# Performance work log

Hardware: AMD Instinct MI355X
Metric: run time of the kernel (lower is better)

Reference implementation:

```python
import jax, jax.numpy as jnp
import numpy as np

B, T, C, H = 4, 2048, 1024, 8
D = C // H


def _rope_tables(t, d, base=10000.0):
    inv = 1.0 / (base ** (jnp.arange(0, d, 2, dtype=jnp.float32) / d))
    freqs = jnp.outer(jnp.arange(t, dtype=jnp.float32), inv)  # (T, D/2)
    cos = jnp.concatenate([jnp.cos(freqs)] * 2, axis=-1)  # (T, D)
    sin = jnp.concatenate([jnp.sin(freqs)] * 2, axis=-1)
    return cos, sin


def _apply_rope(x, cos, sin):
    # x: (B,H,T,D); rotate-half RoPE
    d2 = x.shape[-1] // 2
    x1, x2 = x[..., :d2], x[..., d2:]
    rot = jnp.concatenate([-x2, x1], axis=-1)
    return x * cos + rot * sin


def setup_inputs() -> dict:
    key = jax.random.key(0)
    ks = jax.random.split(key, 8)
    x = jax.random.normal(ks[0], (B, T, C), jnp.float32)
    w = lambda k: jax.random.normal(k, (C, C), jnp.float32) * 0.02
    # trigram directions: 8 sign patterns in {-1,+1}^3, L2-normalized (as in get_trigrams + F.normalize)
    signs = np.array([[(1 if (i >> b) & 1 else -1) for b in range(3)] for i in range(8)], np.float32)
    head_dirs = jnp.asarray(signs / np.sqrt(3.0))
    return {
        'x': x,
        'Wq': w(ks[1]), 'Wk': w(ks[2]), 'Wv': w(ks[3]), 'Wo': w(ks[4]),
        'ln_g': jnp.ones((C,), jnp.float32), 'ln_b': jnp.zeros((C,), jnp.float32),
        'head_scales': jax.random.normal(ks[5], (H,), jnp.float32) * 0.1,
        'head_dirs': head_dirs,
    }


def reference(x, Wq, Wk, Wv, Wo, ln_g, ln_b, head_scales, head_dirs):
    b, t, c = x.shape
    h = head_dirs.shape[0]
    d = c // h
    scale = 1.0 / jnp.sqrt(jnp.asarray(d, x.dtype))
    # pre-LN
    mu = jnp.mean(x, axis=-1, keepdims=True)
    var = jnp.mean((x - mu) ** 2, axis=-1, keepdims=True)
    xn = (x - mu) * jax.lax.rsqrt(var + 1e-5) * ln_g + ln_b
    q = (xn @ Wq.T).reshape(b, t, h, d).transpose(0, 2, 1, 3)  # (B,H,T,D)
    k = (xn @ Wk.T).reshape(b, t, h, d).transpose(0, 2, 1, 3)
    v = (xn @ Wv.T).reshape(b, t, h, d).transpose(0, 2, 1, 3)
    cos, sin = _rope_tables(t, d)
    q = _apply_rope(q, cos, sin)
    k = _apply_rope(k, cos, sin)
    causal = jnp.tril(jnp.ones((t, t), bool))
    # standard causal SDPA
    scores = jnp.einsum('bhqd,bhkd->bhqk', q, k) * scale
    scores = jnp.where(causal, scores, -jnp.inf)
    attn = jax.nn.softmax(scores, axis=-1)
    out = jnp.einsum('bhqk,bhkd->bhqd', attn, v)
    # trigram geometric bias attention (rank-1 logits from first 3 dims)
    qp = jnp.einsum('bhtd,hd->bht', q[..., :3], head_dirs)
    kp = jnp.einsum('bhtd,hd->bht', k[..., :3], head_dirs)
    geo = qp[..., :, None] * kp[..., None, :]  # (B,H,T,T)
    geo = jnp.where(causal, geo, -jnp.inf)
    geo_attn = jax.nn.softmax(geo, axis=-1)
    geo_out = jnp.einsum('bhqk,bhkd->bhqd', geo_attn, v)
    out = out + head_scales[None, :, None, None] * jax.lax.stop_gradient(geo_out - out)
    out = out.transpose(0, 2, 1, 3).reshape(b, t, c) @ Wo.T
    return x + out
```

## Files before the change

### kernel.cpp

```cpp
#include <hip/hip_runtime.h>
#include <hip/hip_bf16.h>
#include <stdint.h>

#define BB 4
#define TT 2048
#define CC 1024
#define HH 8
#define DD 128

typedef unsigned short u16;
typedef unsigned int u32;
typedef unsigned long long u64;
typedef __attribute__((ext_vector_type(4))) float f32x4;
typedef __attribute__((ext_vector_type(16))) float f32x16;
typedef __attribute__((ext_vector_type(8))) __bf16 bf16x8;

__device__ __forceinline__ float bf2f(u16 u){ u32 x=((u32)u)<<16; float f; __builtin_memcpy(&f,&x,4); return f; }
__device__ __forceinline__ u16 f2bf(float f){ u32 x; __builtin_memcpy(&x,&f,4); x += 0x7fffu + ((x>>16)&1u); return (u16)(x>>16); }

__device__ __forceinline__ void gload16(const void* g, void* l){
  __builtin_amdgcn_global_load_lds((const __attribute__((address_space(1))) u32*)g,
                                   (__attribute__((address_space(3))) u32*)l, 16, 0, 0);
}
__device__ __forceinline__ f32x4 mfma16(bf16x8 a, bf16x8 b, f32x4 c){
  return __builtin_amdgcn_mfma_f32_16x16x32_bf16(a,b,c,0,0,0);
}
__device__ __forceinline__ f32x16 mfma32(bf16x8 a, bf16x8 b, f32x16 c){
  return __builtin_amdgcn_mfma_f32_32x32x16_bf16(a,b,c,0,0,0);
}
__device__ __forceinline__ u32 cvtpk(float lo, float hi){
  u32 r; asm("v_cvt_pk_bf16_f32 %0, %1, %2" : "=v"(r) : "v"(lo), "v"(hi)); return r;
}
__device__ __forceinline__ void pl32swap(u32& d, u32& s){
  asm volatile("v_permlane32_swap_b32 %0, %1" : "+v"(d), "+v"(s));
}
union FRAG { u32 u[4]; bf16x8 v; };

__global__ void ln_k(const float* __restrict__ x, const float* __restrict__ g,
                     const float* __restrict__ bta, u16* __restrict__ xn){
  int row = blockIdx.x, tid = threadIdx.x;
  const float4 v = ((const float4*)(x + (size_t)row*CC))[tid];
  float s = v.x+v.y+v.z+v.w;
  float ss = v.x*v.x+v.y*v.y+v.z*v.z+v.w*v.w;
  #pragma unroll
  for(int m=1;m<64;m<<=1){ s += __shfl_xor(s,m); ss += __shfl_xor(ss,m); }
  __shared__ float red[8];
  if((tid&63)==0){ red[tid>>6]=s; red[4+(tid>>6)]=ss; }
  __syncthreads();
  float ts = red[0]+red[1]+red[2]+red[3];
  float tss = red[4]+red[5]+red[6]+red[7];
  float mu = ts*(1.0f/CC);
  float rs = rsqrtf(tss*(1.0f/CC) - mu*mu + 1e-5f);
  int c0 = tid*4;
  ushort4 o;
  o.x = f2bf((v.x-mu)*rs*g[c0+0]+bta[c0+0]);
  o.y = f2bf((v.y-mu)*rs*g[c0+1]+bta[c0+1]);
  o.z = f2bf((v.z-mu)*rs*g[c0+2]+bta[c0+2]);
  o.w = f2bf((v.w-mu)*rs*g[c0+3]+bta[c0+3]);
  ((ushort4*)(xn + (size_t)row*CC))[tid] = o;
}

__global__ void wconv_k(const float* __restrict__ wq, const float* __restrict__ wk,
                        const float* __restrict__ wv, const float* __restrict__ wo,
                        u16* __restrict__ out){
  int i = blockIdx.x*256 + threadIdx.x;
  int sel = i>>18;
  const float* src = sel==0?wq: sel==1?wk: sel==2?wv:wo;
  float4 v = ((const float4*)src)[i & 262143];
  ushort4 o; o.x=f2bf(v.x); o.y=f2bf(v.y); o.z=f2bf(v.z); o.w=f2bf(v.w);
  ((ushort4*)out)[i] = o;
}

__global__ void rope_tab_k(float* __restrict__ cosT, float* __restrict__ sinT){
  int i = blockIdx.x*256 + threadIdx.x;
  int t = i>>6, j = i&63;
  float inv = powf(10000.0f, -(float)(2*j)*(1.0f/128.0f));
  float a = (float)t * inv;
  cosT[i] = cosf(a);
  sinT[i] = sinf(a);
}

__global__ void qpkp_k(const u16* __restrict__ Qb, const u16* __restrict__ Kb,
                       const float* __restrict__ dirs, const float* __restrict__ cosT,
                       const float* __restrict__ sinT, float* __restrict__ qp, float* __restrict__ kp){
  int idx = blockIdx.x*256 + threadIdx.x;
  int b = idx>>14, rem = idx & 16383;
  int h = rem>>11, t = rem & 2047;
  size_t base = ((size_t)(b*TT + t))*CC + h*DD;
  float qv = 0.f, kv = 0.f;
  #pragma unroll
  for(int d=0; d<3; d++){
    float c = cosT[t*64+d], s = sinT[t*64+d];
    float dr = dirs[h*3+d];
    qv += (bf2f(Qb[base+d])*c - bf2f(Qb[base+d+64])*s) * dr;
    kv += (bf2f(Kb[base+d])*c - bf2f(Kb[base+d+64])*s) * dr;
  }
  qp[idx] = qv; kp[idx] = kv;
}

__global__ void ropepack_k(u16* __restrict__ Qb, const u16* __restrict__ Kb,
                           u16* __restrict__ KF,
                           const float* __restrict__ cosT, const float* __restrict__ sinT){
  int bt = blockIdx.x, tid = threadIdx.x;
  int b = bt>>11, t = bt & (TT-1);
  int ks = t>>5, k31 = t&31;
  #pragma unroll
  for(int pp=0; pp<4; pp++){
    int p = tid*4+pp;
    int h = p>>6, d = p&63;
    size_t i1 = (size_t)bt*CC + h*DD + d;
    float c = cosT[t*64+d], s = sinT[t*64+d];
    float q1 = bf2f(Qb[i1]), q2 = bf2f(Qb[i1+64]);
    Qb[i1]    = f2bf(q1*c - q2*s);
    Qb[i1+64] = f2bf(q2*c + q1*s);
    float k1 = bf2f(Kb[i1]), k2 = bf2f(Kb[i1+64]);
    u16 kr1 = f2bf(k1*c - k2*s);
    u16 kr2 = f2bf(k2*c + k1*s);
    int bh = b*HH + h;
    int d2 = d + 64;
    size_t o1 = (((size_t)(bh*64 + ks)*8) + (d >>4))*512 + (((d >>3)&1)*32 + k31)*8 + (d &7);
    size_t o2 = (((size_t)(bh*64 + ks)*8) + (d2>>4))*512 + (((d2>>3)&1)*32 + k31)*8 + (d2&7);
    KF[o1] = kr1;
    KF[o2] = kr2;
  }
}

template<int MODE>
__global__ __launch_bounds__(256) void gemm_k(const u16* __restrict__ A, const u16* __restrict__ W,
                                              u16* __restrict__ outb, float* __restrict__ outf,
                                              const float* __restrict__ resid){
  __shared__ __align__(16) u16 As[128*64];
  __shared__ __align__(16) u16 Bs[128*64];
  const int K = CC;
  int m0 = blockIdx.x*128, n0 = blockIdx.y*128;
  int tid = threadIdx.x, w = tid>>6, l = tid&63;
  int li = l&15, lg = l>>4;
  int wm = w>>1, wn = w&1;
  f32x4 acc[4][4] = {};
  for(int k0=0; k0<K; k0+=64){
    #pragma unroll
    for(int i=0;i<4;i++){
      int L = (w*4+i)*1024 + l*16;
      int row = L>>7;
      int colb = (L&127) ^ ((row&7)<<4);
      gload16(A + ((size_t)(m0+row)*K + k0 + (colb>>1)), (char*)As + (w*4+i)*1024);
      gload16(W + ((size_t)(n0+row)*K + k0 + (colb>>1)), (char*)Bs + (w*4+i)*1024);
    }
    __syncthreads();
    #pragma unroll
    for(int kc=0;kc<2;kc++){
      bf16x8 af[4], bfr[4];
      #pragma unroll
      for(int mi=0;mi<4;mi++){
        int row = wm*64 + mi*16 + li;
        int colb = (kc*64 + lg*16) ^ ((row&7)<<4);
        af[mi] = *(const bf16x8*)((const char*)As + row*128 + colb);
      }
      #pragma unroll
      for(int ni=0;ni<4;ni++){
        int row = wn*64 + ni*16 + li;
        int colb = (kc*64 + lg*16) ^ ((row&7)<<4);
        bfr[ni] = *(const bf16x8*)((const char*)Bs + row*128 + colb);
      }
      #pragma unroll
      for(int mi=0;mi<4;mi++){
        #pragma unroll
        for(int ni=0;ni<4;ni++)
          acc[mi][ni] = mfma16(af[mi], bfr[ni], acc[mi][ni]);
      }
    }
    __syncthreads();
  }
  #pragma unroll
  for(int mi=0;mi<4;mi++){
    #pragma unroll
    for(int ni=0;ni<4;ni++){
      #pragma unroll
      for(int r=0;r<4;r++){
        int row = m0 + wm*64 + mi*16 + lg*4 + r;
        int col = n0 + wn*64 + ni*16 + li;
        float v = acc[mi][ni][r];
        if(MODE==0){
          outb[(size_t)row*CC + col] = f2bf(v);
        } else if(MODE==4){
          int t = row & 2047, b = row>>11;
          int h = col>>7, d = col&127;
          int bh = b*HH + h;
          size_t o = (((size_t)(bh*64 + (t>>5))*8) + (d>>5)*2 + ((t>>4)&1))*512
                     + (((t>>3)&1)*32 + (d&31))*8 + (t&7);
          outb[o] = f2bf(v);
        } else {
          size_t o = (size_t)row*CC + col;
          outf[o] = v + resid[o];
        }
      }
    }
  }
}

__global__ __launch_bounds__(128,2) void attn_k(const u16* __restrict__ Q, const u16* __restrict__ KF,
                                                const u16* __restrict__ VF, const float* __restrict__ qp,
                                                const float* __restrict__ kp, const float* __restrict__ hs,
                                                u16* __restrict__ outp){
  int bid = blockIdx.x;
  int xcd = bid&7, r = bid>>3;
  int bh = xcd*4 + (r&3);
  int strip = 31 - (r>>2);
  int b = bh>>3, h = bh&7;
  int tid = threadIdx.x, w = tid>>6, l = tid&63;
  int l5 = l>>5, q31 = l&31;
  int q0 = strip*64 + w*32;
  int q  = q0 + q31;
  int nsub = (q0>>5) + 1;

  bf16x8 qf[8];
  {
    const u16* qbase = Q + ((size_t)(b*TT + q)*CC + h*DD);
    #pragma unroll
    for(int db=0;db<8;db++) qf[db] = *(const bf16x8*)(qbase + db*16 + l5*8);
  }
  const float L2E = 1.442695040888963f;
  const float sl2 = 0.08838834764831845f * L2E;
  bf16x8 qpf;
  {
    float qs = qp[(size_t)bh*TT + q] * L2E;
    u16 qh = f2bf(qs); float qhf = bf2f(qh);
    u16 ql = f2bf(qs - qhf);
    FRAG fq; fq.u[0] = l5? 0u : ((u32)qh | ((u32)qh<<16));
    fq.u[1] = l5? 0u : (u32)ql; fq.u[2]=0; fq.u[3]=0;
    qpf = fq.v;
  }

  const u16* kfp = KF + (size_t)bh*64*4096 + (size_t)l*8;
  const u16* vfp = VF + (size_t)bh*64*4096 + (size_t)l*8;
  const float* kpp = kp + (size_t)bh*TT + q31;

  float m1=-__builtin_inff(), l1=0.f, m2=-__builtin_inff(), l2=0.f;
  f32x16 a1[4] = {}, a2[4] = {};
  const f32x16 zf = {};

  for(int is=0; is<nsub; ++is){
    int ksub = is*32;

    bf16x8 kf0 = *(const bf16x8*)(kfp + 0*512);
    bf16x8 kf1 = *(const bf16x8*)(kfp + 1*512);
    bf16x8 kf2 = *(const bf16x8*)(kfp + 2*512);
    bf16x8 kf3 = *(const bf16x8*)(kfp + 3*512);
    bf16x8 kf4 = *(const bf16x8*)(kfp + 4*512);
    bf16x8 kf5 = *(const bf16x8*)(kfp + 5*512);
    bf16x8 kf6 = *(const bf16x8*)(kfp + 6*512);
    bf16x8 kf7 = *(const bf16x8*)(kfp + 7*512);

    f32x16 s0 = zf, s1a = zf;
    __builtin_amdgcn_s_setprio(1);
    s0  = mfma32(kf0, qf[0], s0);  s1a = mfma32(kf1, qf[1], s1a);
    s0  = mfma32(kf2, qf[2], s0);  s1a = mfma32(kf3, qf[3], s1a);
    s0  = mfma32(kf4, qf[4], s0);  s1a = mfma32(kf5, qf[5], s1a);
    s0  = mfma32(kf6, qf[6], s0);  s1a = mfma32(kf7, qf[7], s1a);
    __builtin_amdgcn_s_setprio(0);

    f32x16 gg;
    {
      float kpv = kpp[ksub];
      u16 kh = f2bf(kpv); float khf = bf2f(kh);
      u16 kl = f2bf(kpv - khf);
      FRAG fk; fk.u[0] = l5? 0u : ((u32)kh | ((u32)kl<<16));
      fk.u[1] = l5? 0u : (u32)kh; fk.u[2]=0; fk.u[3]=0;
      gg = mfma32(fk.v, qpf, zf);
    }

    float sv[16], gv[16];
    #pragma unroll
    for(int rr=0;rr<16;rr++){ sv[rr] = (s0[rr]+s1a[rr])*sl2; gv[rr] = gg[rr]; }
    if(ksub + 31 > q0){
      #pragma unroll
      for(int rr=0;rr<16;rr++){
        int kg = ksub + (rr&3) + 8*(rr>>2) + 4*l5;
        if(kg > q){ sv[rr] = -__builtin_inff(); gv[rr] = -__builtin_inff(); }
      }
    }

    float mx=-__builtin_inff(), gx=-__builtin_inff();
    #pragma unroll
    for(int rr=0;rr<16;rr++){ mx = fmaxf(mx, sv[rr]); gx = fmaxf(gx, gv[rr]); }
    mx = fmaxf(mx, __shfl_xor(mx,32));
    gx = fmaxf(gx, __shfl_xor(gx,32));
    if(__ballot((mx > m1+8.f) | (gx > m2+8.f))){
      float mn1 = fmaxf(m1,mx), mn2 = fmaxf(m2,gx);
      float c1 = exp2f(m1-mn1), c2 = exp2f(m2-mn2);
      l1 *= c1; l2 *= c2; m1 = mn1; m2 = mn2;
      #pragma unroll
      for(int dt=0;dt<4;dt++){ a1[dt] *= c1; a2[dt] *= c2; }
    }
    float rs1=0.f, rs2=0.f;
    float e1[16], e2[16];
    #pragma unroll
    for(int rr=0;rr<16;rr++){
      e1[rr] = exp2f(sv[rr] - m1); rs1 += e1[rr];
      e2[rr] = exp2f(gv[rr] - m2); rs2 += e2[rr];
    }
    rs1 += __shfl_xor(rs1,32); rs2 += __shfl_xor(rs2,32);
    l1 += rs1; l2 += rs2;

    u32 P1[8], P2[8];
    #pragma unroll
    for(int m=0;m<8;m++){ P1[m] = cvtpk(e1[2*m], e1[2*m+1]); P2[m] = cvtpk(e2[2*m], e2[2*m+1]); }
    pl32swap(P1[0],P1[2]); pl32swap(P1[1],P1[3]); pl32swap(P1[4],P1[6]); pl32swap(P1[5],P1[7]);
    pl32swap(P2[0],P2[2]); pl32swap(P2[1],P2[3]); pl32swap(P2[4],P2[6]); pl32swap(P2[5],P2[7]);

    #pragma unroll
    for(int kb2=0;kb2<2;kb2++){
      FRAG f1, f2;
      #pragma unroll
      for(int j2=0;j2<4;j2++){ f1.u[j2] = P1[kb2*4+j2]; f2.u[j2] = P2[kb2*4+j2]; }
      bf16x8 pb1 = f1.v, pb2 = f2.v;
      bf16x8 vf0 = *(const bf16x8*)(vfp + (0+kb2)*512);
      bf16x8 vf1 = *(const bf16x8*)(vfp + (2+kb2)*512);
      bf16x8 vf2 = *(const bf16x8*)(vfp + (4+kb2)*512);
      bf16x8 vf3 = *(const bf16x8*)(vfp + (6+kb2)*512);
      __builtin_amdgcn_s_setprio(1);
      a1[0] = mfma32(vf0, pb1, a1[0]);  a2[0] = mfma32(vf0, pb2, a2[0]);
      a1[1] = mfma32(vf1, pb1, a1[1]);  a2[1] = mfma32(vf1, pb2, a2[1]);
      a1[2] = mfma32(vf2, pb1, a1[2]);  a2[2] = mfma32(vf2, pb2, a2[2]);
      a1[3] = mfma32(vf3, pb1, a1[3]);  a2[3] = mfma32(vf3, pb2, a2[3]);
      __builtin_amdgcn_s_setprio(0);
    }
    kfp += 4096; vfp += 4096;
  }

  float rl1 = 1.0f/l1, rl2 = 1.0f/l2;
  float sh = hs[h];
  u16* obase = outp + (size_t)(b*TT + q)*CC + h*DD;
  #pragma unroll
  for(int dt=0;dt<4;dt++){
    #pragma unroll
    for(int m=0;m<8;m++){
      float oa1 = a1[dt][2*m]*rl1,   oa2 = a2[dt][2*m]*rl2;
      float ob1 = a1[dt][2*m+1]*rl1, ob2 = a2[dt][2*m+1]*rl2;
      float oa = oa1 + sh*(oa2-oa1);
      float ob = ob1 + sh*(ob2-ob1);
      int d = dt*32 + (2*m&3) + 8*(m>>1) + 4*l5;
      *(u32*)(obase + d) = cvtpk(oa, ob);
    }
  }
}

extern "C" void kernel_launch(void* const* d_in, const int* in_sizes, int n_in,
                              void* d_out, int out_size, void* d_ws, size_t ws_size,
                              hipStream_t stream){
  (void)in_sizes; (void)n_in; (void)out_size; (void)ws_size;
  const float* x   = (const float*)d_in[0];
  const float* Wq  = (const float*)d_in[1];
  const float* Wk  = (const float*)d_in[2];
  const float* Wv  = (const float*)d_in[3];
  const float* Wo  = (const float*)d_in[4];
  const float* lng = (const float*)d_in[5];
  const float* lnb = (const float*)d_in[6];
  const float* hsc = (const float*)d_in[7];
  const float* hdr = (const float*)d_in[8];

  char* ws = (char*)d_ws;
  const size_t MB = 1048576;
  u16* xn   = (u16*)ws;
  u16* wbf  = (u16*)(ws + 16*MB);
  u16* Qb   = (u16*)(ws + 24*MB);
  u16* Kb   = (u16*)(ws + 40*MB);
  u16* VF   = (u16*)(ws + 56*MB);
  u16* KF   = (u16*)(ws + 72*MB);
  float* cosT = (float*)(ws + 88*MB);
  float* sinT = cosT + 131072;
  float* qp   = sinT + 131072;
  float* kp   = qp + 65536;

  ln_k<<<8192,256,0,stream>>>(x, lng, lnb, xn);
  wconv_k<<<4096,256,0,stream>>>(Wq,Wk,Wv,Wo,wbf);
  rope_tab_k<<<512,256,0,stream>>>(cosT,sinT);
  gemm_k<0><<<dim3(64,8),256,0,stream>>>(xn, wbf,          Qb, nullptr, nullptr);
  gemm_k<0><<<dim3(64,8),256,0,stream>>>(xn, wbf+1048576,  Kb, nullptr, nullptr);
  gemm_k<4><<<dim3(64,8),256,0,stream>>>(xn, wbf+2097152,  VF, nullptr, nullptr);
  qpkp_k<<<256,256,0,stream>>>(Qb,Kb,hdr,cosT,sinT,qp,kp);
  ropepack_k<<<8192,128,0,stream>>>(Qb,Kb,KF,cosT,sinT);
  attn_k<<<1024,128,0,stream>>>(Qb,KF,VF,qp,kp,hsc,xn);
  gemm_k<2><<<dim3(64,8),256,0,stream>>>(xn, wbf+3145728, nullptr, (float*)d_out, x);
}
```

Measured before the change: 276.3 us.

## Balance causal attention work by pairing query tiles and splitting keys across waves

Each block now handles query tile p and its mirror 63-p instead of a 64-row strip. Wave 0 processes tile p fully, then the first part of the keys for tile 63-p, while wave 1 processes the remaining keys of tile 63-p. The two partial softmax states are merged through shared memory with a split-softmax rescale. This evens out the causal triangle so every wave does about the same number of key steps, removing the tail imbalance, at the cost of LDS traffic, a barrier and extra merge arithmetic.

```diff
diff --git a/kernel.cpp b/kernel.cpp
--- a/kernel.cpp
+++ b/kernel.cpp
@@ -198,21 +198,20 @@
   }
 }
 
-__global__ __launch_bounds__(128,2) void attn_k(const u16* __restrict__ Q, const u16* __restrict__ KF,
-                                                const u16* __restrict__ VF, const float* __restrict__ qp,
-                                                const float* __restrict__ kp, const float* __restrict__ hs,
-                                                u16* __restrict__ outp){
-  int bid = blockIdx.x;
-  int xcd = bid&7, r = bid>>3;
-  int bh = xcd*4 + (r&3);
-  int strip = 31 - (r>>2);
-  int b = bh>>3, h = bh&7;
-  int tid = threadIdx.x, w = tid>>6, l = tid&63;
-  int l5 = l>>5, q31 = l&31;
-  int q0 = strip*64 + w*32;
-  int q  = q0 + q31;
-  int nsub = (q0>>5) + 1;
-
+struct SegState { float m1, l1, m2, l2; f32x16 a1[4]; f32x16 a2[4]; };
+
+__device__ __forceinline__ void run_seg(int t, int klo, int khi, int bh, int b, int h,
+                                        int l5, int q31,
+                                        const u16* __restrict__ Q, const u16* __restrict__ KF,
+                                        const u16* __restrict__ VF, const float* __restrict__ qp,
+                                        const float* __restrict__ kp, SegState& S){
+  const f32x16 zf = {};
+  S.m1 = -__builtin_inff(); S.l1 = 0.f; S.m2 = -__builtin_inff(); S.l2 = 0.f;
+  #pragma unroll
+  for(int dt=0;dt<4;dt++){ S.a1[dt] = zf; S.a2[dt] = zf; }
+  if(khi <= klo) return;
+
+  int q0 = t*32, q = q0 + q31;
   bf16x8 qf[8];
   {
     const u16* qbase = Q + ((size_t)(b*TT + q)*CC + h*DD);
@@ -230,16 +229,11 @@
     fq.u[1] = l5? 0u : (u32)ql; fq.u[2]=0; fq.u[3]=0;
     qpf = fq.v;
   }
-
-  const u16* kfp = KF + (size_t)bh*64*4096 + (size_t)l*8;
-  const u16* vfp = VF + (size_t)bh*64*4096 + (size_t)l*8;
+  const u16* kfp = KF + (size_t)bh*64*4096 + (size_t)klo*4096 + (size_t)(q31 + 32*l5)*8;
+  const u16* vfp = VF + (size_t)bh*64*4096 + (size_t)klo*4096 + (size_t)(q31 + 32*l5)*8;
   const float* kpp = kp + (size_t)bh*TT + q31;
 
-  float m1=-__builtin_inff(), l1=0.f, m2=-__builtin_inff(), l2=0.f;
-  f32x16 a1[4] = {}, a2[4] = {};
-  const f32x16 zf = {};
-
-  for(int is=0; is<nsub; ++is){
+  for(int is=klo; is<khi; ++is){
     int ksub = is*32;
 
     bf16x8 kf0 = *(const bf16x8*)(kfp + 0*512);
@@ -285,22 +279,22 @@
     for(int rr=0;rr<16;rr++){ mx = fmaxf(mx, sv[rr]); gx = fmaxf(gx, gv[rr]); }
     mx = fmaxf(mx, __shfl_xor(mx,32));
     gx = fmaxf(gx, __shfl_xor(gx,32));
-    if(__ballot((mx > m1+8.f) | (gx > m2+8.f))){
-      float mn1 = fmaxf(m1,mx), mn2 = fmaxf(m2,gx);
-      float c1 = exp2f(m1-mn1), c2 = exp2f(m2-mn2);
-      l1 *= c1; l2 *= c2; m1 = mn1; m2 = mn2;
-      #pragma unroll
-      for(int dt=0;dt<4;dt++){ a1[dt] *= c1; a2[dt] *= c2; }
+    if(__ballot((mx > S.m1+8.f) | (gx > S.m2+8.f))){
+      float mn1 = fmaxf(S.m1,mx), mn2 = fmaxf(S.m2,gx);
+      float c1 = exp2f(S.m1-mn1), c2 = exp2f(S.m2-mn2);
+      S.l1 *= c1; S.l2 *= c2; S.m1 = mn1; S.m2 = mn2;
+      #pragma unroll
+      for(int dt=0;dt<4;dt++){ S.a1[dt] *= c1; S.a2[dt] *= c2; }
     }
     float rs1=0.f, rs2=0.f;
     float e1[16], e2[16];
     #pragma unroll
     for(int rr=0;rr<16;rr++){
-      e1[rr] = exp2f(sv[rr] - m1); rs1 += e1[rr];
-      e2[rr] = exp2f(gv[rr] - m2); rs2 += e2[rr];
+      e1[rr] = exp2f(sv[rr] - S.m1); rs1 += e1[rr];
+      e2[rr] = exp2f(gv[rr] - S.m2); rs2 += e2[rr];
     }
     rs1 += __shfl_xor(rs1,32); rs2 += __shfl_xor(rs2,32);
-    l1 += rs1; l2 += rs2;
+    S.l1 += rs1; S.l2 += rs2;
 
     u32 P1[8], P2[8];
     #pragma unroll
@@ -319,28 +313,90 @@
       bf16x8 vf2 = *(const bf16x8*)(vfp + (4+kb2)*512);
       bf16x8 vf3 = *(const bf16x8*)(vfp + (6+kb2)*512);
       __builtin_amdgcn_s_setprio(1);
-      a1[0] = mfma32(vf0, pb1, a1[0]);  a2[0] = mfma32(vf0, pb2, a2[0]);
-      a1[1] = mfma32(vf1, pb1, a1[1]);  a2[1] = mfma32(vf1, pb2, a2[1]);
-      a1[2] = mfma32(vf2, pb1, a1[2]);  a2[2] = mfma32(vf2, pb2, a2[2]);
-      a1[3] = mfma32(vf3, pb1, a1[3]);  a2[3] = mfma32(vf3, pb2, a2[3]);
+      S.a1[0] = mfma32(vf0, pb1, S.a1[0]);  S.a2[0] = mfma32(vf0, pb2, S.a2[0]);
+      S.a1[1] = mfma32(vf1, pb1, S.a1[1]);  S.a2[1] = mfma32(vf1, pb2, S.a2[1]);
+      S.a1[2] = mfma32(vf2, pb1, S.a1[2]);  S.a2[2] = mfma32(vf2, pb2, S.a2[2]);
+      S.a1[3] = mfma32(vf3, pb1, S.a1[3]);  S.a2[3] = mfma32(vf3, pb2, S.a2[3]);
       __builtin_amdgcn_s_setprio(0);
     }
     kfp += 4096; vfp += 4096;
   }
-
-  float rl1 = 1.0f/l1, rl2 = 1.0f/l2;
+}
+
+__global__ __launch_bounds__(128,2) void attn_k(const u16* __restrict__ Q, const u16* __restrict__ KF,
+                                                const u16* __restrict__ VF, const float* __restrict__ qp,
+                                                const float* __restrict__ kp, const float* __restrict__ hs,
+                                                u16* __restrict__ outp){
+  __shared__ __align__(16) float lp1[4*64*16];
+  __shared__ __align__(16) float lp2[4*64*16];
+  __shared__ float lml[32*4];
+  int bid = blockIdx.x;
+  int xcd = bid&7, r = bid>>3;
+  int bh = xcd*4 + (r&3);
+  int p = r>>2;
+  int b = bh>>3, h = bh&7;
+  int tid = threadIdx.x, w = tid>>6, l = tid&63;
+  int l5 = l>>5, q31 = l&31;
   float sh = hs[h];
-  u16* obase = outp + (size_t)(b*TT + q)*CC + h*DD;
-  #pragma unroll
-  for(int dt=0;dt<4;dt++){
-    #pragma unroll
-    for(int m=0;m<8;m++){
-      float oa1 = a1[dt][2*m]*rl1,   oa2 = a2[dt][2*m]*rl2;
-      float ob1 = a1[dt][2*m+1]*rl1, ob2 = a2[dt][2*m+1]*rl2;
-      float oa = oa1 + sh*(oa2-oa1);
-      float ob = ob1 + sh*(ob2-ob1);
-      int d = dt*32 + (2*m&3) + 8*(m>>1) + 4*l5;
-      *(u32*)(obase + d) = cvtpk(oa, ob);
+
+  SegState S;
+  if(w==0){
+    run_seg(p, 0, p+1, bh, b, h, l5, q31, Q, KF, VF, qp, kp, S);
+    {
+      float rl1 = 1.0f/S.l1, rl2 = 1.0f/S.l2;
+      int q = p*32 + q31;
+      u16* obase = outp + (size_t)(b*TT + q)*CC + h*DD;
+      #pragma unroll
+      for(int dt=0;dt<4;dt++){
+        #pragma unroll
+        for(int m=0;m<8;m++){
+          float oa1 = S.a1[dt][2*m]*rl1,   oa2 = S.a2[dt][2*m]*rl2;
+          float ob1 = S.a1[dt][2*m+1]*rl1, ob2 = S.a2[dt][2*m+1]*rl2;
+          float oa = oa1 + sh*(oa2-oa1);
+          float ob = ob1 + sh*(ob2-ob1);
+          int d = dt*32 + (2*m&3) + 8*(m>>1) + 4*l5;
+          *(u32*)(obase + d) = cvtpk(oa, ob);
+        }
+      }
+    }
+    run_seg(63-p, 0, 31-p, bh, b, h, l5, q31, Q, KF, VF, qp, kp, S);
+    #pragma unroll
+    for(int dt=0;dt<4;dt++){
+      *(f32x16*)&lp1[(dt*64 + l)*16] = S.a1[dt];
+      *(f32x16*)&lp2[(dt*64 + l)*16] = S.a2[dt];
+    }
+    if(l5==0){
+      lml[q31*4+0] = S.m1; lml[q31*4+1] = S.l1;
+      lml[q31*4+2] = S.m2; lml[q31*4+3] = S.l2;
+    }
+    __syncthreads();
+  } else {
+    run_seg(63-p, 31-p, 64-p, bh, b, h, l5, q31, Q, KF, VF, qp, kp, S);
+    __syncthreads();
+    float mA1 = lml[q31*4+0], lA1 = lml[q31*4+1];
+    float mA2 = lml[q31*4+2], lA2 = lml[q31*4+3];
+    float M1 = fmaxf(mA1, S.m1), M2 = fmaxf(mA2, S.m2);
+    float wA1 = exp2f(mA1-M1), wB1 = exp2f(S.m1-M1);
+    float wA2 = exp2f(mA2-M2), wB2 = exp2f(S.m2-M2);
+    float r1 = 1.0f/(wA1*lA1 + wB1*S.l1);
+    float r2 = 1.0f/(wA2*lA2 + wB2*S.l2);
+    int q = (63-p)*32 + q31;
+    u16* obase = outp + (size_t)(b*TT + q)*CC + h*DD;
+    #pragma unroll
+    for(int dt=0;dt<4;dt++){
+      f32x16 pa1 = *(const f32x16*)&lp1[(dt*64 + l)*16];
+      f32x16 pa2 = *(const f32x16*)&lp2[(dt*64 + l)*16];
+      #pragma unroll
+      for(int m=0;m<8;m++){
+        float oa1 = (wA1*pa1[2*m]   + wB1*S.a1[dt][2*m])*r1;
+        float ob1 = (wA1*pa1[2*m+1] + wB1*S.a1[dt][2*m+1])*r1;
+        float oa2 = (wA2*pa2[2*m]   + wB2*S.a2[dt][2*m])*r2;
+        float ob2 = (wA2*pa2[2*m+1] + wB2*S.a2[dt][2*m+1])*r2;
+        float oa = oa1 + sh*(oa2-oa1);
+        float ob = ob1 + sh*(ob2-ob1);
+        int d = dt*32 + (2*m&3) + 8*(m>>1) + 4*l5;
+        *(u32*)(obase + d) = cvtpk(oa, ob);
+      }
     }
   }
 }
```

New measurement: 231.6 us. 16.2% less time.
